# Performance work log

Measured on AMD Instinct MI355X. Metric: run time of the kernel, lower is better.

Reference implementation:

```python
import jax, jax.numpy as jnp
import numpy as np

SH_DIM = 9                      # (sh_deg+1)^2, sh_deg=2
DATA_DIM = SH_DIM * 3 + 1       # 28
FINE = 8
COARSE = 32
RADIUS = 1.3
NUM_ATOMS = 16
BATCH = 128
STEP = (RADIUS * 2.0 / COARSE / FINE) / 2.0   # fine_voxel_len / 2
N_INTRS = COARSE * 3 * 2 * FINE               # 1536


def sh_encode(dirs):
    # degree-2 real spherical harmonics bases, [.., 9]
    x, y, z = dirs[..., 0], dirs[..., 1], dirs[..., 2]
    C0 = 0.28209479177387814
    C1 = 0.4886025119029199
    C2 = (1.0925484305920792, -1.0925484305920792, 0.31539156525252005,
          -1.0925484305920792, 0.5462742152960396)
    return jnp.stack([
        jnp.full_like(x, C0), -C1 * y, C1 * z, -C1 * x,
        C2[0] * x * y, C2[1] * y * z, C2[2] * (2.0 * z * z - x * x - y * y),
        C2[3] * x * z, C2[4] * (x * x - y * y)], axis=-1)


def dict_interp(grid, atoms, pts):
    # pts: [N,3] normalized to [0,1). grid: [COARSE^3, A]. atoms: [FINE^3, A, D].
    # coarse voxel -> dictionary coefficients; trilinear interp of atoms inside it.
    cpos = pts * COARSE
    cidx = jnp.clip(jnp.floor(cpos), 0, COARSE - 1)
    ci = cidx.astype(jnp.int32)
    coeff = grid[(ci[:, 0] * COARSE + ci[:, 1]) * COARSE + ci[:, 2]]  # [N, A]
    local = cpos - cidx                       # [0,1) within coarse voxel
    fpos = local * FINE - 0.5
    f0f = jnp.floor(fpos)
    w = fpos - f0f                            # trilinear weights
    f0 = f0f.astype(jnp.int32)
    out = jnp.zeros((pts.shape[0], DATA_DIM), dtype=pts.dtype)
    for dx in (0, 1):
        for dy in (0, 1):
            for dz in (0, 1):
                ix = jnp.clip(f0[:, 0] + dx, 0, FINE - 1)
                iy = jnp.clip(f0[:, 1] + dy, 0, FINE - 1)
                iz = jnp.clip(f0[:, 2] + dz, 0, FINE - 1)
                wt = ((w[:, 0] if dx else 1.0 - w[:, 0]) *
                      (w[:, 1] if dy else 1.0 - w[:, 1]) *
                      (w[:, 2] if dz else 1.0 - w[:, 2]))
                vals = jnp.einsum('na,nad->nd', coeff, atoms[(ix * FINE + iy) * FINE + iz])
                out = out + wt[:, None] * vals
    return out


def setup_inputs() -> dict:
    key = jax.random.key(0)
    k1, k2, k3, k4 = jax.random.split(key, 4)
    rays_o = jnp.array([0.0, 0.0, -2.0 * RADIUS]) + 0.05 * jax.random.normal(k1, (BATCH, 3), jnp.float32)
    d = 0.25 * jax.random.normal(k2, (BATCH, 3), jnp.float32) + jnp.array([0.0, 0.0, 1.0])
    rays_d = d / jnp.linalg.norm(d, axis=-1, keepdims=True)
    grid = 0.01 * jax.random.normal(k3, (COARSE ** 3, NUM_ATOMS), jnp.float32)
    atoms_sh = jax.random.uniform(k4, (FINE ** 3, NUM_ATOMS, DATA_DIM - 1), jnp.float32)
    atoms = jnp.concatenate([atoms_sh, jnp.full((FINE ** 3, NUM_ATOMS, 1), 0.01, jnp.float32)], -1)
    return {"rays_o": rays_o, "rays_d": rays_d, "grid": grid, "atoms": atoms, "grid_id": 0}


def reference(rays_o, rays_d, grid, atoms, grid_id):
    B = rays_o.shape[0]
    # ---- sample_proposal (no-grad in original) ----
    off_pos = (RADIUS - rays_o) / rays_d
    off_neg = (-RADIUS - rays_o) / rays_d
    start = jnp.max(jnp.minimum(off_pos, off_neg), axis=-1, keepdims=True)
    steps = jnp.arange(N_INTRS, dtype=rays_o.dtype)[None, :]
    intersections = jax.lax.stop_gradient(start + steps * STEP)        # [B, 1536]
    tsec = intersections[:, :-1]                                       # [B, M]
    M = N_INTRS - 1
    pts = rays_o[:, None, :] + tsec[:, :, None] * rays_d[:, None, :]   # [B, M, 3]
    mask = jnp.all((pts > -RADIUS) & (pts < RADIUS), axis=-1)          # [B, M]
    pts_n = jnp.clip((pts + RADIUS) / (2.0 * RADIUS), 0.0, 1.0 - 1e-6)
    pts_n = jax.lax.stop_gradient(pts_n).reshape(-1, 3)
    # ---- dictionary interpolation (computed densely, zeroed by mask) ----
    data = dict_interp(grid, atoms, pts_n).reshape(B, M, DATA_DIM)
    sigma = jax.nn.relu(jnp.where(mask, data[..., -1], 0.0))           # [B, M]
    # ---- sigma -> alpha / weights ----
    dists = (intersections[:, 1:] - intersections[:, :-1]) * jnp.linalg.norm(rays_d, axis=-1, keepdims=True)
    alpha = 1.0 - jnp.exp(-sigma * dists)
    trans = jnp.concatenate([jnp.ones((B, 1), alpha.dtype),
                             jnp.cumprod(1.0 - alpha + 1e-10, axis=-1)[:, :-1]], axis=-1)
    abs_light = alpha * trans                                          # [B, M]
    # ---- SH -> rgb, composite ----
    sh_mult = sh_encode(rays_d)[:, None, None, :]                      # [B,1,1,9]
    sh = data[..., :-1].reshape(B, M, 3, SH_DIM)
    rgb_raw = jnp.where(mask[..., None], jnp.sum(sh_mult * sh, axis=-1), 0.0)  # [B,M,3]
    rgb = jnp.sum(abs_light[..., None] * jax.nn.sigmoid(rgb_raw), axis=1)
    rgb = rgb + (1.0 - jnp.sum(abs_light, axis=-1))[:, None]           # white background
    depth = jnp.sum(abs_light * tsec, axis=-1)
    return rgb, alpha, depth
```

## Files before the change

### kernel.cpp

```cpp
#include <hip/hip_runtime.h>
#include <hip/hip_fp16.h>

typedef unsigned int u32;
typedef _Float16 half2v __attribute__((ext_vector_type(2)));
union H2 { u32 u; half2v v; };

#define MSAMP 1535
#define NS 1024
#define RADF 1.3f
#define STEPF ((float)(1.3 * 2.0 / 32.0 / 8.0 / 2.0))

__global__ __launch_bounds__(256) void k_t(const float* __restrict__ atoms,
                                           __half* __restrict__ wst) {
    int o = blockIdx.x * 256 + threadIdx.x;
    float v = atoms[o];
    int cell = o / 448;
    int r = o - cell * 448;
    int a = r / 28;
    int d = r - a * 28;
    int s = d >> 2, j = d & 3;
    wst[s * 32768 + cell * 64 + j * 16 + a] = __float2half(v);
}

__global__ __launch_bounds__(512) void k_p1(const float* __restrict__ ro,
                                            const float* __restrict__ rd,
                                            const float* __restrict__ gridf,
                                            const __half* __restrict__ wst,
                                            __half* __restrict__ raw) {
    __shared__ __half hl[512 * 68];
    int bx = blockIdx.x;
    int s  = bx >> 6;
    int pr = bx & 63;
    int tid = threadIdx.x;
    int ray = pr * 2 + (tid >> 8);
    int q   = tid & 255;

    {
        const uint4* src = (const uint4*)(wst + s * 32768);
#pragma unroll
        for (int it = 0; it < 8; it++) {
            int idx = it * 512 + tid;
            uint4 v = src[idx];
            int cell  = idx >> 3;
            int inner = (idx & 7) << 3;
            *(uint2*)&hl[cell * 68 + inner]     = make_uint2(v.x, v.y);
            *(uint2*)&hl[cell * 68 + inner + 4] = make_uint2(v.z, v.w);
        }
    }
    __syncthreads();

    float ox = ro[ray * 3 + 0], oy = ro[ray * 3 + 1], oz = ro[ray * 3 + 2];
    float dx = rd[ray * 3 + 0], dy = rd[ray * 3 + 1], dz = rd[ray * 3 + 2];
    float a0 = ( RADF - ox) / dx, b0 = (-RADF - ox) / dx;
    float a1 = ( RADF - oy) / dy, b1 = (-RADF - oy) / dy;
    float a2 = ( RADF - oz) / dz, b2 = (-RADF - oz) / dz;
    float st = fmaxf(fmaxf(fminf(a0, b0), fminf(a1, b1)), fminf(a2, b2));

#pragma unroll
    for (int k = 0; k < 4; k++) {
        int m = q + k * 256;
        float t = st + (float)m * STEPF;
        float px = ox + t * dx, py = oy + t * dy, pz = oz + t * dz;
        bool inb = (px > -RADF) && (px < RADF) && (py > -RADF) && (py < RADF)
                && (pz > -RADF) && (pz < RADF);
        if (!inb) continue;

        const float inv2R = 1.0f / 2.6f;
        float pnx = fminf(fmaxf((px + RADF) * inv2R, 0.0f), 0.999999f);
        float pny = fminf(fmaxf((py + RADF) * inv2R, 0.0f), 0.999999f);
        float pnz = fminf(fmaxf((pz + RADF) * inv2R, 0.0f), 0.999999f);

        float cpx = pnx * 32.0f, cpy = pny * 32.0f, cpz = pnz * 32.0f;
        float cfx = floorf(cpx), cfy = floorf(cpy), cfz = floorf(cpz);
        int cix = (int)cfx, ciy = (int)cfy, ciz = (int)cfz;

        float fpx = (cpx - cfx) * 8.0f - 0.5f;
        float fpy = (cpy - cfy) * 8.0f - 0.5f;
        float fpz = (cpz - cfz) * 8.0f - 0.5f;
        float ffx = floorf(fpx), ffy = floorf(fpy), ffz = floorf(fpz);
        int f0x = (int)ffx, f0y = (int)ffy, f0z = (int)ffz;
        float wx = fpx - ffx, wy = fpy - ffy, wz = fpz - ffz;

        int ixa[2] = { max(f0x, 0), min(f0x + 1, 7) };
        int iya[2] = { max(f0y, 0), min(f0y + 1, 7) };
        int iza[2] = { max(f0z, 0), min(f0z + 1, 7) };
        float wxa[2] = { 1.0f - wx, wx };
        float wya[2] = { 1.0f - wy, wy };
        float wza[2] = { 1.0f - wz, wz };

        half2v ch[8];
        {
            const float4* cp = (const float4*)(gridf + (((cix * 32 + ciy) * 32 + ciz) << 4));
            float4 c0 = cp[0], c1 = cp[1], c2 = cp[2], c3 = cp[3];
            ch[0] = half2v{(_Float16)c0.x, (_Float16)c0.y};
            ch[1] = half2v{(_Float16)c0.z, (_Float16)c0.w};
            ch[2] = half2v{(_Float16)c1.x, (_Float16)c1.y};
            ch[3] = half2v{(_Float16)c1.z, (_Float16)c1.w};
            ch[4] = half2v{(_Float16)c2.x, (_Float16)c2.y};
            ch[5] = half2v{(_Float16)c2.z, (_Float16)c2.w};
            ch[6] = half2v{(_Float16)c3.x, (_Float16)c3.y};
            ch[7] = half2v{(_Float16)c3.z, (_Float16)c3.w};
        }

        float acc[4] = {0.0f, 0.0f, 0.0f, 0.0f};

#pragma unroll
        for (int cx = 0; cx < 2; cx++)
#pragma unroll
        for (int cy = 0; cy < 2; cy++)
#pragma unroll
        for (int cz = 0; cz < 2; cz++) {
            float wt = wxa[cx] * wya[cy] * wza[cz];
            int cb = ((ixa[cx] * 8 + iya[cy]) * 8 + iza[cz]) * 68;
            float dd[4] = {0.0f, 0.0f, 0.0f, 0.0f};
#pragma unroll
            for (int g = 0; g < 4; g++) {
#pragma unroll
                for (int j = 0; j < 4; j++) {
                    uint2 qv = *(const uint2*)&hl[cb + j * 16 + g * 4];
                    H2 a0h, a1h; a0h.u = qv.x; a1h.u = qv.y;
                    dd[j] = __builtin_amdgcn_fdot2(a0h.v, ch[2 * g],     dd[j], false);
                    dd[j] = __builtin_amdgcn_fdot2(a1h.v, ch[2 * g + 1], dd[j], false);
                }
            }
#pragma unroll
            for (int j = 0; j < 4; j++) acc[j] = fmaf(wt, dd[j], acc[j]);
        }

        __half2 p0 = __floats2half2_rn(acc[0], acc[1]);
        __half2 p1 = __floats2half2_rn(acc[2], acc[3]);
        uint2 pv;
        pv.x = *(u32*)&p0;
        pv.y = *(u32*)&p1;
        *(uint2*)&raw[(ray * NS + m) * 28 + s * 4] = pv;
    }
}

__global__ __launch_bounds__(1024) void k_p2(const float* __restrict__ ro,
                                             const float* __restrict__ rd,
                                             const __half* __restrict__ raw,
                                             float* __restrict__ rgb_out,
                                             float* __restrict__ alpha_out,
                                             float* __restrict__ depth_out) {
    int ray = blockIdx.x;
    int t = threadIdx.x;
    int lane = t & 63, wave = t >> 6;

    int abase = ray * MSAMP;
    if (NS + t < MSAMP) alpha_out[abase + NS + t] = 0.0f;

    float ox = ro[ray * 3 + 0], oy = ro[ray * 3 + 1], oz = ro[ray * 3 + 2];
    float dx = rd[ray * 3 + 0], dy = rd[ray * 3 + 1], dz = rd[ray * 3 + 2];
    float a0 = ( RADF - ox) / dx, b0 = (-RADF - ox) / dx;
    float a1 = ( RADF - oy) / dy, b1 = (-RADF - oy) / dy;
    float a2 = ( RADF - oz) / dz, b2 = (-RADF - oz) / dz;
    float st = fmaxf(fmaxf(fminf(a0, b0), fminf(a1, b1)), fminf(a2, b2));
    float nrm = sqrtf(dx * dx + dy * dy + dz * dz);

    float shm[9];
    shm[0] = 0.28209479177387814f;
    shm[1] = -0.4886025119029199f * dy;
    shm[2] =  0.4886025119029199f * dz;
    shm[3] = -0.4886025119029199f * dx;
    shm[4] =  1.0925484305920792f * dx * dy;
    shm[5] = -1.0925484305920792f * dy * dz;
    shm[6] =  0.31539156525252005f * (2.0f * dz * dz - dx * dx - dy * dy);
    shm[7] = -1.0925484305920792f * dx * dz;
    shm[8] =  0.5462742152960396f * (dx * dx - dy * dy);

    int m = t;
    float tm = st + (float)m * STEPF;
    float px = ox + tm * dx, py = oy + tm * dy, pz = oz + tm * dz;
    bool inb = (px > -RADF) && (px < RADF) && (py > -RADF) && (py < RADF)
            && (pz > -RADF) && (pz < RADF);
    float alpha = 0.0f, r0 = 0.0f, r1 = 0.0f, r2 = 0.0f;
    if (inb) {
        const __half* rp = raw + (ray * NS + m) * 28;
        float v[28];
#pragma unroll
        for (int i = 0; i < 7; i++) {
            uint2 qv = *(const uint2*)(rp + i * 4);
            __half2 h0 = *(__half2*)&qv.x;
            __half2 h1 = *(__half2*)&qv.y;
            float2 f0v = __half22float2(h0);
            float2 f1v = __half22float2(h1);
            v[i*4+0] = f0v.x; v[i*4+1] = f0v.y; v[i*4+2] = f1v.x; v[i*4+3] = f1v.y;
        }
        float sigma = fmaxf(v[27], 0.0f);
        alpha = 1.0f - __expf(-sigma * STEPF * nrm);
        float rr[3];
#pragma unroll
        for (int cch = 0; cch < 3; cch++) {
            float sdot = 0.0f;
#pragma unroll
            for (int j = 0; j < 9; j++) sdot = fmaf(shm[j], v[cch * 9 + j], sdot);
            rr[cch] = 1.0f / (1.0f + __expf(-sdot));
        }
        r0 = rr[0]; r1 = rr[1]; r2 = rr[2];
    }
    alpha_out[abase + m] = alpha;

    float p = 1.0f - alpha + 1e-10f;

    float incl = p;
#pragma unroll
    for (int off = 1; off < 64; off <<= 1) {
        float vv = __shfl_up(incl, off);
        if (lane >= off) incl *= vv;
    }
    __shared__ float wprod[16];
    if (lane == 63) wprod[wave] = incl;
    __syncthreads();
    float excl = __shfl_up(incl, 1);
    if (lane == 0) excl = 1.0f;
    for (int w = 0; w < 16; w++) if (w < wave) excl *= wprod[w];

    float trans = excl;
    float w_ = alpha * trans;
    float ra = w_ * r0, ga = w_ * r1, ba = w_ * r2;
    float da = w_ * tm, wsum = w_;

    float vals[5] = { ra, ga, ba, da, wsum };
    __shared__ float wred[16][5];
#pragma unroll
    for (int i = 0; i < 5; i++) {
        float v = vals[i];
        v += __shfl_xor(v, 1);  v += __shfl_xor(v, 2);  v += __shfl_xor(v, 4);
        v += __shfl_xor(v, 8);  v += __shfl_xor(v, 16); v += __shfl_xor(v, 32);
        if (lane == 0) wred[wave][i] = v;
    }
    __syncthreads();
    if (t == 0) {
        float res[5];
#pragma unroll
        for (int i = 0; i < 5; i++) {
            float r_ = 0.0f;
            for (int w = 0; w < 16; w++) r_ += wred[w][i];
            res[i] = r_;
        }
        float omw = 1.0f - res[4];
        rgb_out[ray * 3 + 0] = res[0] + omw;
        rgb_out[ray * 3 + 1] = res[1] + omw;
        rgb_out[ray * 3 + 2] = res[2] + omw;
        depth_out[ray] = res[3];
    }
}

extern "C" void kernel_launch(void* const* d_in, const int* in_sizes, int n_in,
                              void* d_out, int out_size, void* d_ws, size_t ws_size,
                              hipStream_t stream) {
    const float* ro    = (const float*)d_in[0];
    const float* rd    = (const float*)d_in[1];
    const float* grid  = (const float*)d_in[2];
    const float* atoms = (const float*)d_in[3];
    int B = in_sizes[0] / 3;

    __half* wst = (__half*)d_ws;
    __half* raw = (__half*)((char*)d_ws + 458752);

    float* out       = (float*)d_out;
    float* rgb_out   = out;
    float* alpha_out = out + B * 3;
    float* depth_out = out + B * 3 + B * MSAMP;

    hipLaunchKernelGGL(k_t,  dim3(896), dim3(256), 0, stream, atoms, wst);
    hipLaunchKernelGGL(k_p1, dim3(448), dim3(512), 0, stream, ro, rd, grid, wst, raw);
    hipLaunchKernelGGL(k_p2, dim3(B),   dim3(1024), 0, stream, ro, rd, raw,
                       rgb_out, alpha_out, depth_out);
}
```

Baseline: 87.58 us.

## Fuse SH projection into interpolation kernel with atomic float4 accumulation and half grid

The interpolation kernel now projects each 4-wide output slice onto the per-ray SH basis and atomically adds the result into a per-sample float4 of r, g, b and sigma. This replaces the 28-channel half intermediate buffer. The prep kernel also converts the coarse grid to fp16 once and zeroes the accumulator, so grid gathers in the main kernel are half the size. The compositing kernel then reads one float4 per sample instead of 28 halves. In exchange it adds fp32 global atomics, up to two per slice per sample, plus extra prep traffic for the grid conversion and accumulator zeroing on every call.

```diff
diff --git a/kernel.cpp b/kernel.cpp
--- a/kernel.cpp
+++ b/kernel.cpp
@@ -9,24 +9,37 @@
 #define NS 1024
 #define RADF 1.3f
 #define STEPF ((float)(1.3 * 2.0 / 32.0 / 8.0 / 2.0))
+#define NATOMS 229376
+#define NGRID  524288
 
 __global__ __launch_bounds__(256) void k_t(const float* __restrict__ atoms,
-                                           __half* __restrict__ wst) {
+                                           const float* __restrict__ grid,
+                                           __half* __restrict__ wst,
+                                           __half* __restrict__ gridh,
+                                           float4* __restrict__ acc4) {
     int o = blockIdx.x * 256 + threadIdx.x;
-    float v = atoms[o];
-    int cell = o / 448;
-    int r = o - cell * 448;
-    int a = r / 28;
-    int d = r - a * 28;
-    int s = d >> 2, j = d & 3;
-    wst[s * 32768 + cell * 64 + j * 16 + a] = __float2half(v);
+    if (o < NATOMS) {
+        float v = atoms[o];
+        int cell = o / 448;
+        int r = o - cell * 448;
+        int a = r / 28;
+        int d = r - a * 28;
+        int s = d >> 2, j = d & 3;
+        wst[s * 32768 + cell * 64 + j * 16 + a] = __float2half(v);
+    } else if (o < NATOMS + NGRID) {
+        int i = o - NATOMS;
+        gridh[i] = __float2half(grid[i]);
+    } else {
+        int i = o - (NATOMS + NGRID);
+        acc4[i] = make_float4(0.0f, 0.0f, 0.0f, 0.0f);
+    }
 }
 
 __global__ __launch_bounds__(512) void k_p1(const float* __restrict__ ro,
                                             const float* __restrict__ rd,
-                                            const float* __restrict__ gridf,
+                                            const __half* __restrict__ gridh,
                                             const __half* __restrict__ wst,
-                                            __half* __restrict__ raw) {
+                                            float* __restrict__ acc4) {
     __shared__ __half hl[512 * 68];
     int bx = blockIdx.x;
     int s  = bx >> 6;
@@ -55,107 +68,6 @@
     float a1 = ( RADF - oy) / dy, b1 = (-RADF - oy) / dy;
     float a2 = ( RADF - oz) / dz, b2 = (-RADF - oz) / dz;
     float st = fmaxf(fmaxf(fminf(a0, b0), fminf(a1, b1)), fminf(a2, b2));
-
-#pragma unroll
-    for (int k = 0; k < 4; k++) {
-        int m = q + k * 256;
-        float t = st + (float)m * STEPF;
-        float px = ox + t * dx, py = oy + t * dy, pz = oz + t * dz;
-        bool inb = (px > -RADF) && (px < RADF) && (py > -RADF) && (py < RADF)
-                && (pz > -RADF) && (pz < RADF);
-        if (!inb) continue;
-
-        const float inv2R = 1.0f / 2.6f;
-        float pnx = fminf(fmaxf((px + RADF) * inv2R, 0.0f), 0.999999f);
-        float pny = fminf(fmaxf((py + RADF) * inv2R, 0.0f), 0.999999f);
-        float pnz = fminf(fmaxf((pz + RADF) * inv2R, 0.0f), 0.999999f);
-
-        float cpx = pnx * 32.0f, cpy = pny * 32.0f, cpz = pnz * 32.0f;
-        float cfx = floorf(cpx), cfy = floorf(cpy), cfz = floorf(cpz);
-        int cix = (int)cfx, ciy = (int)cfy, ciz = (int)cfz;
-
-        float fpx = (cpx - cfx) * 8.0f - 0.5f;
-        float fpy = (cpy - cfy) * 8.0f - 0.5f;
-        float fpz = (cpz - cfz) * 8.0f - 0.5f;
-        float ffx = floorf(fpx), ffy = floorf(fpy), ffz = floorf(fpz);
-        int f0x = (int)ffx, f0y = (int)ffy, f0z = (int)ffz;
-        float wx = fpx - ffx, wy = fpy - ffy, wz = fpz - ffz;
-
-        int ixa[2] = { max(f0x, 0), min(f0x + 1, 7) };
-        int iya[2] = { max(f0y, 0), min(f0y + 1, 7) };
-        int iza[2] = { max(f0z, 0), min(f0z + 1, 7) };
-        float wxa[2] = { 1.0f - wx, wx };
-        float wya[2] = { 1.0f - wy, wy };
-        float wza[2] = { 1.0f - wz, wz };
-
-        half2v ch[8];
-        {
-            const float4* cp = (const float4*)(gridf + (((cix * 32 + ciy) * 32 + ciz) << 4));
-            float4 c0 = cp[0], c1 = cp[1], c2 = cp[2], c3 = cp[3];
-            ch[0] = half2v{(_Float16)c0.x, (_Float16)c0.y};
-            ch[1] = half2v{(_Float16)c0.z, (_Float16)c0.w};
-            ch[2] = half2v{(_Float16)c1.x, (_Float16)c1.y};
-            ch[3] = half2v{(_Float16)c1.z, (_Float16)c1.w};
-            ch[4] = half2v{(_Float16)c2.x, (_Float16)c2.y};
-            ch[5] = half2v{(_Float16)c2.z, (_Float16)c2.w};
-            ch[6] = half2v{(_Float16)c3.x, (_Float16)c3.y};
-            ch[7] = half2v{(_Float16)c3.z, (_Float16)c3.w};
-        }
-
-        float acc[4] = {0.0f, 0.0f, 0.0f, 0.0f};
-
-#pragma unroll
-        for (int cx = 0; cx < 2; cx++)
-#pragma unroll
-        for (int cy = 0; cy < 2; cy++)
-#pragma unroll
-        for (int cz = 0; cz < 2; cz++) {
-            float wt = wxa[cx] * wya[cy] * wza[cz];
-            int cb = ((ixa[cx] * 8 + iya[cy]) * 8 + iza[cz]) * 68;
-            float dd[4] = {0.0f, 0.0f, 0.0f, 0.0f};
-#pragma unroll
-            for (int g = 0; g < 4; g++) {
-#pragma unroll
-                for (int j = 0; j < 4; j++) {
-                    uint2 qv = *(const uint2*)&hl[cb + j * 16 + g * 4];
-                    H2 a0h, a1h; a0h.u = qv.x; a1h.u = qv.y;
-                    dd[j] = __builtin_amdgcn_fdot2(a0h.v, ch[2 * g],     dd[j], false);
-                    dd[j] = __builtin_amdgcn_fdot2(a1h.v, ch[2 * g + 1], dd[j], false);
-                }
-            }
-#pragma unroll
-            for (int j = 0; j < 4; j++) acc[j] = fmaf(wt, dd[j], acc[j]);
-        }
-
-        __half2 p0 = __floats2half2_rn(acc[0], acc[1]);
-        __half2 p1 = __floats2half2_rn(acc[2], acc[3]);
-        uint2 pv;
-        pv.x = *(u32*)&p0;
-        pv.y = *(u32*)&p1;
-        *(uint2*)&raw[(ray * NS + m) * 28 + s * 4] = pv;
-    }
-}
-
-__global__ __launch_bounds__(1024) void k_p2(const float* __restrict__ ro,
-                                             const float* __restrict__ rd,
-                                             const __half* __restrict__ raw,
-                                             float* __restrict__ rgb_out,
-                                             float* __restrict__ alpha_out,
-                                             float* __restrict__ depth_out) {
-    int ray = blockIdx.x;
-    int t = threadIdx.x;
-    int lane = t & 63, wave = t >> 6;
-
-    int abase = ray * MSAMP;
-    if (NS + t < MSAMP) alpha_out[abase + NS + t] = 0.0f;
-
-    float ox = ro[ray * 3 + 0], oy = ro[ray * 3 + 1], oz = ro[ray * 3 + 2];
-    float dx = rd[ray * 3 + 0], dy = rd[ray * 3 + 1], dz = rd[ray * 3 + 2];
-    float a0 = ( RADF - ox) / dx, b0 = (-RADF - ox) / dx;
-    float a1 = ( RADF - oy) / dy, b1 = (-RADF - oy) / dy;
-    float a2 = ( RADF - oz) / dz, b2 = (-RADF - oz) / dz;
-    float st = fmaxf(fmaxf(fminf(a0, b0), fminf(a1, b1)), fminf(a2, b2));
-    float nrm = sqrtf(dx * dx + dy * dy + dz * dz);
 
     float shm[9];
     shm[0] = 0.28209479177387814f;
@@ -168,36 +80,127 @@
     shm[7] = -1.0925484305920792f * dx * dz;
     shm[8] =  0.5462742152960396f * (dx * dx - dy * dy);
 
+    float wA[4] = {0,0,0,0}, wB[4] = {0,0,0,0};
+    int chanA = 0, chanB = 0; bool hasB = false;
+    switch (s) {
+        case 0: chanA=0; wA[0]=shm[0]; wA[1]=shm[1]; wA[2]=shm[2]; wA[3]=shm[3]; break;
+        case 1: chanA=0; wA[0]=shm[4]; wA[1]=shm[5]; wA[2]=shm[6]; wA[3]=shm[7]; break;
+        case 2: chanA=0; wA[0]=shm[8];
+                chanB=1; wB[1]=shm[0]; wB[2]=shm[1]; wB[3]=shm[2]; hasB=true; break;
+        case 3: chanA=1; wA[0]=shm[3]; wA[1]=shm[4]; wA[2]=shm[5]; wA[3]=shm[6]; break;
+        case 4: chanA=1; wA[0]=shm[7]; wA[1]=shm[8];
+                chanB=2; wB[2]=shm[0]; wB[3]=shm[1]; hasB=true; break;
+        case 5: chanA=2; wA[0]=shm[2]; wA[1]=shm[3]; wA[2]=shm[4]; wA[3]=shm[5]; break;
+        default: chanA=2; wA[0]=shm[6]; wA[1]=shm[7]; wA[2]=shm[8];
+                chanB=3; wB[3]=1.0f; hasB=true; break;
+    }
+
+#pragma unroll
+    for (int k = 0; k < 4; k++) {
+        int m = q + k * 256;
+        float t = st + (float)m * STEPF;
+        float px = ox + t * dx, py = oy + t * dy, pz = oz + t * dz;
+        bool inb = (px > -RADF) && (px < RADF) && (py > -RADF) && (py < RADF)
+                && (pz > -RADF) && (pz < RADF);
+        if (!inb) continue;
+
+        const float inv2R = 1.0f / 2.6f;
+        float pnx = fminf(fmaxf((px + RADF) * inv2R, 0.0f), 0.999999f);
+        float pny = fminf(fmaxf((py + RADF) * inv2R, 0.0f), 0.999999f);
+        float pnz = fminf(fmaxf((pz + RADF) * inv2R, 0.0f), 0.999999f);
+
+        float cpx = pnx * 32.0f, cpy = pny * 32.0f, cpz = pnz * 32.0f;
+        float cfx = floorf(cpx), cfy = floorf(cpy), cfz = floorf(cpz);
+        int cix = (int)cfx, ciy = (int)cfy, ciz = (int)cfz;
+
+        float fpx = (cpx - cfx) * 8.0f - 0.5f;
+        float fpy = (cpy - cfy) * 8.0f - 0.5f;
+        float fpz = (cpz - cfz) * 8.0f - 0.5f;
+        float ffx = floorf(fpx), ffy = floorf(fpy), ffz = floorf(fpz);
+        int f0x = (int)ffx, f0y = (int)ffy, f0z = (int)ffz;
+        float wx = fpx - ffx, wy = fpy - ffy, wz = fpz - ffz;
+
+        int ixa[2] = { max(f0x, 0), min(f0x + 1, 7) };
+        int iya[2] = { max(f0y, 0), min(f0y + 1, 7) };
+        int iza[2] = { max(f0z, 0), min(f0z + 1, 7) };
+        float wxa[2] = { 1.0f - wx, wx };
+        float wya[2] = { 1.0f - wy, wy };
+        float wza[2] = { 1.0f - wz, wz };
+
+        H2 ch[8];
+        {
+            const uint4* gp = (const uint4*)(gridh + (((cix * 32 + ciy) * 32 + ciz) << 4));
+            uint4 q0 = gp[0], q1 = gp[1];
+            ch[0].u = q0.x; ch[1].u = q0.y; ch[2].u = q0.z; ch[3].u = q0.w;
+            ch[4].u = q1.x; ch[5].u = q1.y; ch[6].u = q1.z; ch[7].u = q1.w;
+        }
+
+        float acc[4] = {0.0f, 0.0f, 0.0f, 0.0f};
+
+#pragma unroll
+        for (int cx = 0; cx < 2; cx++)
+#pragma unroll
+        for (int cy = 0; cy < 2; cy++)
+#pragma unroll
+        for (int cz = 0; cz < 2; cz++) {
+            float wt = wxa[cx] * wya[cy] * wza[cz];
+            int cb = ((ixa[cx] * 8 + iya[cy]) * 8 + iza[cz]) * 68;
+            float dd[4] = {0.0f, 0.0f, 0.0f, 0.0f};
+#pragma unroll
+            for (int g = 0; g < 4; g++) {
+#pragma unroll
+                for (int j = 0; j < 4; j++) {
+                    uint2 qv = *(const uint2*)&hl[cb + j * 16 + g * 4];
+                    H2 a0h, a1h; a0h.u = qv.x; a1h.u = qv.y;
+                    dd[j] = __builtin_amdgcn_fdot2(a0h.v, ch[2 * g].v,     dd[j], false);
+                    dd[j] = __builtin_amdgcn_fdot2(a1h.v, ch[2 * g + 1].v, dd[j], false);
+                }
+            }
+#pragma unroll
+            for (int j = 0; j < 4; j++) acc[j] = fmaf(wt, dd[j], acc[j]);
+        }
+
+        float vA = fmaf(wA[0], acc[0], fmaf(wA[1], acc[1],
+                   fmaf(wA[2], acc[2], wA[3] * acc[3])));
+        int base = (ray * NS + m) * 4;
+        atomicAdd(&acc4[base + chanA], vA);
+        if (hasB) {
+            float vB = fmaf(wB[0], acc[0], fmaf(wB[1], acc[1],
+                       fmaf(wB[2], acc[2], wB[3] * acc[3])));
+            atomicAdd(&acc4[base + chanB], vB);
+        }
+    }
+}
+
+__global__ __launch_bounds__(1024) void k_p2(const float* __restrict__ ro,
+                                             const float* __restrict__ rd,
+                                             const float4* __restrict__ acc4,
+                                             float* __restrict__ rgb_out,
+                                             float* __restrict__ alpha_out,
+                                             float* __restrict__ depth_out) {
+    int ray = blockIdx.x;
+    int t = threadIdx.x;
+    int lane = t & 63, wave = t >> 6;
+
+    int abase = ray * MSAMP;
+    if (NS + t < MSAMP) alpha_out[abase + NS + t] = 0.0f;
+
+    float dx = rd[ray * 3 + 0], dy = rd[ray * 3 + 1], dz = rd[ray * 3 + 2];
+    float ox = ro[ray * 3 + 0], oy = ro[ray * 3 + 1], oz = ro[ray * 3 + 2];
+    float a0 = ( RADF - ox) / dx, b0 = (-RADF - ox) / dx;
+    float a1 = ( RADF - oy) / dy, b1 = (-RADF - oy) / dy;
+    float a2 = ( RADF - oz) / dz, b2 = (-RADF - oz) / dz;
+    float st = fmaxf(fmaxf(fminf(a0, b0), fminf(a1, b1)), fminf(a2, b2));
+    float nrm = sqrtf(dx * dx + dy * dy + dz * dz);
+
     int m = t;
     float tm = st + (float)m * STEPF;
-    float px = ox + tm * dx, py = oy + tm * dy, pz = oz + tm * dz;
-    bool inb = (px > -RADF) && (px < RADF) && (py > -RADF) && (py < RADF)
-            && (pz > -RADF) && (pz < RADF);
-    float alpha = 0.0f, r0 = 0.0f, r1 = 0.0f, r2 = 0.0f;
-    if (inb) {
-        const __half* rp = raw + (ray * NS + m) * 28;
-        float v[28];
-#pragma unroll
-        for (int i = 0; i < 7; i++) {
-            uint2 qv = *(const uint2*)(rp + i * 4);
-            __half2 h0 = *(__half2*)&qv.x;
-            __half2 h1 = *(__half2*)&qv.y;
-            float2 f0v = __half22float2(h0);
-            float2 f1v = __half22float2(h1);
-            v[i*4+0] = f0v.x; v[i*4+1] = f0v.y; v[i*4+2] = f1v.x; v[i*4+3] = f1v.y;
-        }
-        float sigma = fmaxf(v[27], 0.0f);
-        alpha = 1.0f - __expf(-sigma * STEPF * nrm);
-        float rr[3];
-#pragma unroll
-        for (int cch = 0; cch < 3; cch++) {
-            float sdot = 0.0f;
-#pragma unroll
-            for (int j = 0; j < 9; j++) sdot = fmaf(shm[j], v[cch * 9 + j], sdot);
-            rr[cch] = 1.0f / (1.0f + __expf(-sdot));
-        }
-        r0 = rr[0]; r1 = rr[1]; r2 = rr[2];
-    }
+    float4 d4 = acc4[ray * NS + m];
+    float sigma = fmaxf(d4.w, 0.0f);
+    float alpha = 1.0f - __expf(-sigma * STEPF * nrm);
+    float r0 = 1.0f / (1.0f + __expf(-d4.x));
+    float r1 = 1.0f / (1.0f + __expf(-d4.y));
+    float r2 = 1.0f / (1.0f + __expf(-d4.z));
     alpha_out[abase + m] = alpha;
 
     float p = 1.0f - alpha + 1e-10f;
@@ -215,12 +218,8 @@
     if (lane == 0) excl = 1.0f;
     for (int w = 0; w < 16; w++) if (w < wave) excl *= wprod[w];
 
-    float trans = excl;
-    float w_ = alpha * trans;
-    float ra = w_ * r0, ga = w_ * r1, ba = w_ * r2;
-    float da = w_ * tm, wsum = w_;
-
-    float vals[5] = { ra, ga, ba, da, wsum };
+    float w_ = alpha * excl;
+    float vals[5] = { w_ * r0, w_ * r1, w_ * r2, w_ * tm, w_ };
     __shared__ float wred[16][5];
 #pragma unroll
     for (int i = 0; i < 5; i++) {
@@ -255,16 +254,19 @@
     const float* atoms = (const float*)d_in[3];
     int B = in_sizes[0] / 3;
 
-    __half* wst = (__half*)d_ws;
-    __half* raw = (__half*)((char*)d_ws + 458752);
+    __half* wst   = (__half*)d_ws;
+    __half* gridh = (__half*)((char*)d_ws + 458752);
+    float*  acc4  = (float*)((char*)d_ws + 458752 + 1048576);
 
     float* out       = (float*)d_out;
     float* rgb_out   = out;
     float* alpha_out = out + B * 3;
     float* depth_out = out + B * 3 + B * MSAMP;
 
-    hipLaunchKernelGGL(k_t,  dim3(896), dim3(256), 0, stream, atoms, wst);
-    hipLaunchKernelGGL(k_p1, dim3(448), dim3(512), 0, stream, ro, rd, grid, wst, raw);
-    hipLaunchKernelGGL(k_p2, dim3(B),   dim3(1024), 0, stream, ro, rd, raw,
-                       rgb_out, alpha_out, depth_out);
-}
+    hipLaunchKernelGGL(k_t,  dim3(884736 / 256), dim3(256), 0, stream,
+                       atoms, grid, wst, gridh, (float4*)acc4);
+    hipLaunchKernelGGL(k_p1, dim3(448), dim3(512), 0, stream,
+                       ro, rd, gridh, wst, acc4);
+    hipLaunchKernelGGL(k_p2, dim3(B), dim3(1024), 0, stream,
+                       ro, rd, (const float4*)acc4, rgb_out, alpha_out, depth_out);
+}
```

Result: no change. 88.58 us (+1.1%).
